# Performance work log

Measured on AMD Instinct MI355X. Metric: run time of the kernel, lower is better.

Reference implementation:

```python
import jax, jax.numpy as jnp
import numpy as np


def _mlp(x, W0, b0, W1, b1, W2, b2, W3, b3):
    # nlayers=4 MLP: 3->128->128->128->3 with ReLU between layers
    h = jax.nn.relu(x @ W0 + b0)
    h = jax.nn.relu(h @ W1 + b1)
    h = jax.nn.relu(h @ W2 + b2)
    return h @ W3 + b3


def setup_inputs() -> dict:
    key = jax.random.key(0)
    ks = jax.random.split(key, 8)
    B, Nc, Nt, Dx, Dy, H = 8, 1024, 1024, 3, 32, 128
    s = lambda fan: 1.0 / np.sqrt(fan)
    return {
        "xc": jax.random.normal(ks[0], (B, Nc, Dx), jnp.float32),
        "yc": jax.random.normal(ks[1], (B, Nc, Dy), jnp.float32),
        "xt": jax.random.normal(ks[2], (B, Nt, Dx), jnp.float32),
        "W0": jax.random.normal(ks[3], (Dx, H), jnp.float32) * s(Dx),
        "b0": jnp.zeros((H,), jnp.float32),
        "W1": jax.random.normal(ks[4], (H, H), jnp.float32) * s(H),
        "b1": jnp.zeros((H,), jnp.float32),
        "W2": jax.random.normal(ks[5], (H, H), jnp.float32) * s(H),
        "b2": jnp.zeros((H,), jnp.float32),
        "W3": jax.random.normal(ks[6], (H, Dx), jnp.float32) * s(H),
        "b3": jnp.zeros((Dx,), jnp.float32),
    }


def reference(xc, yc, xt, W0, b0, W1, b1, W2, b2, W3, b3):
    # sigmas: per-target, per-coordinate positive scales  (B, Nt, Dx)
    sig = jnp.exp(_mlp(xt, W0, b0, W1, b1, W2, b2, W3, b3))
    # squared differences (B, Nc, Nt, Dx), scaled and reduced over Dx
    A = (xc[:, :, None, :] - xt[:, None, :, :]) ** 2
    P = -(A * sig[:, None, :, :]).sum(axis=3)        # (B, Nc, Nt)
    S = jax.nn.softmax(P, axis=1)                    # softmax over context
    # weighted average of context values: (B, Nt, Dy)
    return jnp.einsum("bnd,bnt->btd", yc, S)
```

## Files before the change

kernel.cpp:

```cpp
#include <hip/hip_runtime.h>
#include <math.h>

#define BB 8
#define NCC 1024
#define NTT 1024
#define HH 128
#define DYY 32
#define NTB 16
#define LOG2E 1.44269504088896340736f

typedef _Float16 half8 __attribute__((ext_vector_type(8)));
typedef float f32x4 __attribute__((ext_vector_type(4)));

#define HB 0
#define RED 2112
#define WCH 2496
#define SIGL 8192
#define SMEM_SZ 8240
#define CMB 0
#define SL 4224
#define HSTRIDE 132

__global__ __launch_bounds__(512, 2) void k_fused(const float* __restrict__ xc,
                                                  const float* __restrict__ yc,
                                                  const float* __restrict__ xt,
                                                  const float* __restrict__ W0,
                                                  const float* __restrict__ b0,
                                                  const float* __restrict__ W1,
                                                  const float* __restrict__ b1,
                                                  const float* __restrict__ W2,
                                                  const float* __restrict__ b2,
                                                  const float* __restrict__ W3,
                                                  const float* __restrict__ b3,
                                                  float* __restrict__ out) {
    const int tid = threadIdx.x;
    const int phys = blockIdx.x;
    const int bid = (phys & 7) * 64 + (phys >> 3);
    const int t0 = bid * NTB;
    const int b = bid >> 6;
    const int wv = tid >> 6;
    const int lane = tid & 63;

    __shared__ float smem[SMEM_SZ];

    const float4* __restrict__ xcG4 = (const float4*)(xc + (size_t)b * NCC * 3);

    const int jg = tid >> 4;
    const int p = tid & 15;
    const int j0 = jg * 4;
    const int jl4 = (jg & 3) * 4;
    float* hrow = smem + HB + p * HSTRIDE;

    {
        const float* xr = xt + (size_t)(t0 + p) * 3;
        const float x0 = xr[0], x1 = xr[1], x2 = xr[2];
        const float4* W0v = (const float4*)W0;
        const float4 w0a = W0v[jg], w0b = W0v[32 + jg], w0c = W0v[64 + jg];
        const float4 bb0 = ((const float4*)b0)[jg];
        float4 h0;
        h0.x = fmaxf(fmaf(x0, w0a.x, fmaf(x1, w0b.x, fmaf(x2, w0c.x, bb0.x))), 0.f);
        h0.y = fmaxf(fmaf(x0, w0a.y, fmaf(x1, w0b.y, fmaf(x2, w0c.y, bb0.y))), 0.f);
        h0.z = fmaxf(fmaf(x0, w0a.z, fmaf(x1, w0b.z, fmaf(x2, w0c.z, bb0.z))), 0.f);
        h0.w = fmaxf(fmaf(x0, w0a.w, fmaf(x1, w0b.w, fmaf(x2, w0c.w, bb0.w))), 0.f);
        *(float4*)(hrow + j0) = h0;
    }

    const int gWb = (lane >> 2) * 32 + wv * 4 + (lane & 3);
    float* wwb = smem + WCH + wv * 512;
    const float4* __restrict__ W1v = (const float4*)W1;
    const float4* __restrict__ W2v = (const float4*)W2;

    float4 wA0 = W1v[gWb], wA1 = W1v[gWb + 512];
    __syncthreads();

    auto run_layer = [&](const float4* __restrict__ Wv, const float4 bi,
                         float4 r0, float4 r1) -> float4 {
        float a0 = bi.x, a1 = bi.y, a2 = bi.z, a3 = bi.w;
        ((float4*)wwb)[lane] = r0;
        float4 wcur = r1;
#pragma unroll
        for (int c = 0; c < 8; ++c) {
            float4 wnext;
            if (c < 6) wnext = Wv[gWb + (c + 2) * 512];
            if (c < 7) ((float4*)(wwb + ((c + 1) & 1) * 256))[lane] = wcur;
            const float* wbc = wwb + (c & 1) * 256;
#pragma unroll
            for (int q = 0; q < 4; ++q) {
                const float4 ch = *(const float4*)(hrow + c * 16 + q * 4);
                const float4 k0 = *(const float4*)(wbc + (q * 4 + 0) * 16 + jl4);
                const float4 k1 = *(const float4*)(wbc + (q * 4 + 1) * 16 + jl4);
                const float4 k2 = *(const float4*)(wbc + (q * 4 + 2) * 16 + jl4);
                const float4 k3 = *(const float4*)(wbc + (q * 4 + 3) * 16 + jl4);
                a0 = fmaf(ch.x, k0.x, a0);
                a1 = fmaf(ch.x, k0.y, a1);
                a2 = fmaf(ch.x, k0.z, a2);
                a3 = fmaf(ch.x, k0.w, a3);
                a0 = fmaf(ch.y, k1.x, a0);
                a1 = fmaf(ch.y, k1.y, a1);
                a2 = fmaf(ch.y, k1.z, a2);
                a3 = fmaf(ch.y, k1.w, a3);
                a0 = fmaf(ch.z, k2.x, a0);
                a1 = fmaf(ch.z, k2.y, a1);
                a2 = fmaf(ch.z, k2.z, a2);
                a3 = fmaf(ch.z, k2.w, a3);
                a0 = fmaf(ch.w, k3.x, a0);
                a1 = fmaf(ch.w, k3.y, a1);
                a2 = fmaf(ch.w, k3.z, a2);
                a3 = fmaf(ch.w, k3.w, a3);
            }
            wcur = wnext;
        }
        float4 r;
        r.x = fmaxf(a0, 0.f);
        r.y = fmaxf(a1, 0.f);
        r.z = fmaxf(a2, 0.f);
        r.w = fmaxf(a3, 0.f);
        return r;
    };

    float4 oL1 = run_layer(W1v, ((const float4*)b1)[jg], wA0, wA1);
    float4 wB0 = W2v[gWb], wB1 = W2v[gWb + 512];
    __syncthreads();
    *(float4*)(hrow + j0) = oL1;
    __syncthreads();
    float4 oL2 = run_layer(W2v, ((const float4*)b2)[jg], wB0, wB1);

    {
        const float4* W3v = (const float4*)W3;
        const float4 wr0 = W3v[jg * 3 + 0];
        const float4 wr1 = W3v[jg * 3 + 1];
        const float4 wr2 = W3v[jg * 3 + 2];
        float p0 = oL2.x * wr0.x + oL2.y * wr0.w + oL2.z * wr1.z + oL2.w * wr2.y;
        float p1 = oL2.x * wr0.y + oL2.y * wr1.x + oL2.z * wr1.w + oL2.w * wr2.z;
        float p2 = oL2.x * wr0.z + oL2.y * wr1.y + oL2.z * wr2.x + oL2.w * wr2.w;
        p0 += __shfl_xor(p0, 16, 64);
        p0 += __shfl_xor(p0, 32, 64);
        p1 += __shfl_xor(p1, 16, 64);
        p1 += __shfl_xor(p1, 32, 64);
        p2 += __shfl_xor(p2, 16, 64);
        p2 += __shfl_xor(p2, 32, 64);
        if (lane < 16) {
            smem[RED + wv * 48 + lane * 3 + 0] = p0;
            smem[RED + wv * 48 + lane * 3 + 1] = p1;
            smem[RED + wv * 48 + lane * 3 + 2] = p2;
        }
    }
    __syncthreads();
    if (tid < 48) {
        const int r = tid / 3, cix = tid - r * 3;
        float v = b3[cix];
#pragma unroll
        for (int g2 = 0; g2 < 8; ++g2) v += smem[RED + g2 * 48 + r * 3 + cix];
        smem[SIGL + r * 3 + cix] = __expf(v) * LOG2E;
    }
    __syncthreads();

    const int tl = lane & 15;
    const int g = lane >> 4;
    const int sd = lane & 31;
    const int snr = lane >> 5;

    const float s0 = smem[SIGL + tl * 3 + 0];
    const float s1 = smem[SIGL + tl * 3 + 1];
    const float s2 = smem[SIGL + tl * 3 + 2];
    const float* ar = xt + (size_t)(t0 + tl) * 3;
    const float a0 = ar[0], a1 = ar[1], a2 = ar[2];

    float* warena = smem + wv * 1024;
    _Float16* ycT = (_Float16*)warena;
    float* xcw = warena + 640;

    if (lane < 48) {
        float4 tx0 = xcG4[wv * 96 + lane];
        float4 tx1 = xcG4[wv * 96 + 48 + lane];
        ((float4*)xcw)[lane] = tx0;
        ((float4*)xcw)[lane + 48] = tx1;
    }

    const float* ycol = yc + (size_t)b * NCC * DYY + (size_t)(wv * 128) * DYY + sd;
    float ld[16];
#define YLOAD(C)                                                               \
    _Pragma("unroll") for (int q = 0; q < 16; ++q)                             \
        ld[q] = ycol[(size_t)((C) * 32 + (q >> 3) * 16 + snr * 8 + (q & 7)) * DYY];
#define YWRITE()                                                               \
    do {                                                                       \
        _Pragma("unroll") for (int r = 0; r < 2; ++r) {                        \
            half8 pk;                                                          \
            _Pragma("unroll") for (int j = 0; j < 8; ++j)                      \
                pk[j] = (_Float16)ld[r * 8 + j];                               \
            *(half8*)(ycT + sd * 40 + r * 16 + snr * 8) = pk;                  \
        }                                                                      \
    } while (0)

    YLOAD(0);
    YWRITE();

    f32x4 acc0 = {0.f, 0.f, 0.f, 0.f};
    f32x4 acc1 = {0.f, 0.f, 0.f, 0.f};
    float l = 0.f;

#pragma unroll
    for (int c = 0; c < 4; ++c) {
        if (c < 3) YLOAD(c + 1);

        float xv[24];
        {
            const float4* xr4 = (const float4*)(xcw + (c * 32 + g * 8) * 3);
#pragma unroll
            for (int q = 0; q < 6; ++q) *(float4*)(xv + q * 4) = xr4[q];
        }
        half8 af;
#pragma unroll
        for (int i = 0; i < 8; ++i) {
            const float d0 = xv[i * 3 + 0] - a0;
            const float d1 = xv[i * 3 + 1] - a1;
            const float d2 = xv[i * 3 + 2] - a2;
            const float pp = fmaf(s0, d0 * d0, fmaf(s1, d1 * d1, s2 * (d2 * d2)));
            const _Float16 eh = (_Float16)exp2f(-pp);
            af[i] = eh;
            l += (float)eh;
        }
        const half8 bf0 = *(const half8*)(ycT + tl * 40 + g * 8);
        const half8 bf1 = *(const half8*)(ycT + (16 + tl) * 40 + g * 8);
        acc0 = __builtin_amdgcn_mfma_f32_16x16x32_f16(af, bf0, acc0, 0, 0, 0);
        acc1 = __builtin_amdgcn_mfma_f32_16x16x32_f16(af, bf1, acc1, 0, 0, 0);

        if (c < 3) YWRITE();
    }

    l += __shfl_xor(l, 16, 64);
    l += __shfl_xor(l, 32, 64);

    __syncthreads();
#pragma unroll
    for (int r = 0; r < 4; ++r) {
        smem[CMB + wv * 528 + (g * 4 + r) * 33 + tl] = acc0[r];
        smem[CMB + wv * 528 + (g * 4 + r) * 33 + 16 + tl] = acc1[r];
    }
    if (lane < 16) smem[SL + wv * 16 + lane] = l;
    __syncthreads();
    {
        const int t = tid >> 5, d = tid & 31;
        float s = 0.f, ls = 0.f;
#pragma unroll
        for (int w = 0; w < 8; ++w) {
            s += smem[CMB + w * 528 + t * 33 + d];
            ls += smem[SL + w * 16 + t];
        }
        out[(size_t)(t0 + t) * DYY + d] = s / ls;
    }
#undef YLOAD
#undef YWRITE
}

extern "C" void kernel_launch(void* const* d_in, const int* in_sizes, int n_in,
                              void* d_out, int out_size, void* d_ws, size_t ws_size,
                              hipStream_t stream) {
    const float* xc = (const float*)d_in[0];
    const float* yc = (const float*)d_in[1];
    const float* xt = (const float*)d_in[2];
    const float* W0 = (const float*)d_in[3];
    const float* b0 = (const float*)d_in[4];
    const float* W1 = (const float*)d_in[5];
    const float* b1 = (const float*)d_in[6];
    const float* W2 = (const float*)d_in[7];
    const float* b2 = (const float*)d_in[8];
    const float* W3 = (const float*)d_in[9];
    const float* b3 = (const float*)d_in[10];
    float* out = (float*)d_out;

    k_fused<<<dim3(BB * NTT / NTB), dim3(512), 0, stream>>>(xc, yc, xt, W0, b0,
                                                            W1, b1, W2, b2, W3,
                                                            b3, out);
}
```

Measured before the change: 91.90 us.

## Compute hidden MLP layers with split-fp16 MFMA instead of scalar FMA

Replaces the scalar-FMA hidden layers, which staged weights through LDS, with MFMA 16x16x32 f16 instructions. Each fp32 operand is split into a high and a low fp16 part and three MFMAs are issued per chunk to keep accuracy close to fp32. Weights are now read directly from global memory per lane, and hidden activations go back to LDS between layers with extra barriers. The MLP is only a small part of the kernel next to the softmax attention, so the overall effect is likely modest, and the split-fp16 scheme carries a small accuracy risk.

```diff
diff --git a/kernel.cpp b/kernel.cpp
--- a/kernel.cpp
+++ b/kernel.cpp
@@ -14,7 +14,6 @@
 
 #define HB 0
 #define RED 2112
-#define WCH 2496
 #define SIGL 8192
 #define SMEM_SZ 8240
 #define CMB 0
@@ -48,7 +47,6 @@
     const int jg = tid >> 4;
     const int p = tid & 15;
     const int j0 = jg * 4;
-    const int jl4 = (jg & 3) * 4;
     float* hrow = smem + HB + p * HSTRIDE;
 
     {
@@ -64,75 +62,73 @@
         h0.w = fmaxf(fmaf(x0, w0a.w, fmaf(x1, w0b.w, fmaf(x2, w0c.w, bb0.w))), 0.f);
         *(float4*)(hrow + j0) = h0;
     }
-
-    const int gWb = (lane >> 2) * 32 + wv * 4 + (lane & 3);
-    float* wwb = smem + WCH + wv * 512;
-    const float4* __restrict__ W1v = (const float4*)W1;
-    const float4* __restrict__ W2v = (const float4*)W2;
-
-    float4 wA0 = W1v[gWb], wA1 = W1v[gWb + 512];
-    __syncthreads();
-
-    auto run_layer = [&](const float4* __restrict__ Wv, const float4 bi,
-                         float4 r0, float4 r1) -> float4 {
-        float a0 = bi.x, a1 = bi.y, a2 = bi.z, a3 = bi.w;
-        ((float4*)wwb)[lane] = r0;
-        float4 wcur = r1;
-#pragma unroll
-        for (int c = 0; c < 8; ++c) {
-            float4 wnext;
-            if (c < 6) wnext = Wv[gWb + (c + 2) * 512];
-            if (c < 7) ((float4*)(wwb + ((c + 1) & 1) * 256))[lane] = wcur;
-            const float* wbc = wwb + (c & 1) * 256;
-#pragma unroll
-            for (int q = 0; q < 4; ++q) {
-                const float4 ch = *(const float4*)(hrow + c * 16 + q * 4);
-                const float4 k0 = *(const float4*)(wbc + (q * 4 + 0) * 16 + jl4);
-                const float4 k1 = *(const float4*)(wbc + (q * 4 + 1) * 16 + jl4);
-                const float4 k2 = *(const float4*)(wbc + (q * 4 + 2) * 16 + jl4);
-                const float4 k3 = *(const float4*)(wbc + (q * 4 + 3) * 16 + jl4);
-                a0 = fmaf(ch.x, k0.x, a0);
-                a1 = fmaf(ch.x, k0.y, a1);
-                a2 = fmaf(ch.x, k0.z, a2);
-                a3 = fmaf(ch.x, k0.w, a3);
-                a0 = fmaf(ch.y, k1.x, a0);
-                a1 = fmaf(ch.y, k1.y, a1);
-                a2 = fmaf(ch.y, k1.z, a2);
-                a3 = fmaf(ch.y, k1.w, a3);
-                a0 = fmaf(ch.z, k2.x, a0);
-                a1 = fmaf(ch.z, k2.y, a1);
-                a2 = fmaf(ch.z, k2.z, a2);
-                a3 = fmaf(ch.z, k2.w, a3);
-                a0 = fmaf(ch.w, k3.x, a0);
-                a1 = fmaf(ch.w, k3.y, a1);
-                a2 = fmaf(ch.w, k3.z, a2);
-                a3 = fmaf(ch.w, k3.w, a3);
+    __syncthreads();
+
+    {
+        const int mtl = lane & 15;
+        const int mg = lane >> 4;
+        const int jcol = wv * 16 + mtl;
+
+#pragma unroll
+        for (int l = 0; l < 2; ++l) {
+            const float* __restrict__ Wg = (l == 0) ? W1 : W2;
+            const float* __restrict__ bi = (l == 0) ? b1 : b2;
+            f32x4 dac;
+            {
+                const float bj = bi[jcol];
+                dac[0] = bj; dac[1] = bj; dac[2] = bj; dac[3] = bj;
             }
-            wcur = wnext;
-        }
-        float4 r;
-        r.x = fmaxf(a0, 0.f);
-        r.y = fmaxf(a1, 0.f);
-        r.z = fmaxf(a2, 0.f);
-        r.w = fmaxf(a3, 0.f);
-        return r;
-    };
-
-    float4 oL1 = run_layer(W1v, ((const float4*)b1)[jg], wA0, wA1);
-    float4 wB0 = W2v[gWb], wB1 = W2v[gWb + 512];
-    __syncthreads();
-    *(float4*)(hrow + j0) = oL1;
-    __syncthreads();
-    float4 oL2 = run_layer(W2v, ((const float4*)b2)[jg], wB0, wB1);
-
-    {
+            float w[8];
+#pragma unroll
+            for (int i = 0; i < 8; ++i) w[i] = Wg[(mg * 8 + i) * HH + jcol];
+#pragma unroll
+            for (int c = 0; c < 4; ++c) {
+                float wn[8];
+                if (c < 3) {
+#pragma unroll
+                    for (int i = 0; i < 8; ++i)
+                        wn[i] = Wg[((c + 1) * 32 + mg * 8 + i) * HH + jcol];
+                }
+                float hv[8];
+                *(float4*)hv =
+                    *(const float4*)(smem + HB + mtl * HSTRIDE + c * 32 + mg * 8);
+                *(float4*)(hv + 4) =
+                    *(const float4*)(smem + HB + mtl * HSTRIDE + c * 32 + mg * 8 + 4);
+                half8 a0, a1, bf0, bf1;
+#pragma unroll
+                for (int i = 0; i < 8; ++i) {
+                    const _Float16 ah = (_Float16)hv[i];
+                    a0[i] = ah;
+                    a1[i] = (_Float16)(hv[i] - (float)ah);
+                    const _Float16 wh = (_Float16)w[i];
+                    bf0[i] = wh;
+                    bf1[i] = (_Float16)(w[i] - (float)wh);
+                }
+                dac = __builtin_amdgcn_mfma_f32_16x16x32_f16(a0, bf0, dac, 0, 0, 0);
+                dac = __builtin_amdgcn_mfma_f32_16x16x32_f16(a0, bf1, dac, 0, 0, 0);
+                dac = __builtin_amdgcn_mfma_f32_16x16x32_f16(a1, bf0, dac, 0, 0, 0);
+                if (c < 3) {
+#pragma unroll
+                    for (int i = 0; i < 8; ++i) w[i] = wn[i];
+                }
+            }
+            __syncthreads();
+#pragma unroll
+            for (int r = 0; r < 4; ++r)
+                smem[HB + (mg * 4 + r) * HSTRIDE + jcol] = fmaxf(dac[r], 0.f);
+            __syncthreads();
+        }
+    }
+
+    {
+        const float4 o4 = *(const float4*)(hrow + j0);
         const float4* W3v = (const float4*)W3;
         const float4 wr0 = W3v[jg * 3 + 0];
         const float4 wr1 = W3v[jg * 3 + 1];
         const float4 wr2 = W3v[jg * 3 + 2];
-        float p0 = oL2.x * wr0.x + oL2.y * wr0.w + oL2.z * wr1.z + oL2.w * wr2.y;
-        float p1 = oL2.x * wr0.y + oL2.y * wr1.x + oL2.z * wr1.w + oL2.w * wr2.z;
-        float p2 = oL2.x * wr0.z + oL2.y * wr1.y + oL2.z * wr2.x + oL2.w * wr2.w;
+        float p0 = o4.x * wr0.x + o4.y * wr0.w + o4.z * wr1.z + o4.w * wr2.y;
+        float p1 = o4.x * wr0.y + o4.y * wr1.x + o4.z * wr1.w + o4.w * wr2.z;
+        float p2 = o4.x * wr0.z + o4.y * wr1.y + o4.z * wr2.x + o4.w * wr2.w;
         p0 += __shfl_xor(p0, 16, 64);
         p0 += __shfl_xor(p0, 32, 64);
         p1 += __shfl_xor(p1, 16, 64);
```

New measurement: 85.54 us. 1.07x faster.
